# Optimization experiments

Hardware: AMD Instinct MI355X
Metric: run time of the kernel (lower is better)

Reference implementation:

```python
import jax, jax.numpy as jnp
import numpy as np

V, H, B, S, L = 32000, 1024, 128, 256, 2


def setup_inputs() -> dict:
    key = jax.random.key(0)
    ks = jax.random.split(key, 20)
    p = lambda k, shape: (0.02 * jax.random.normal(k, shape)).astype(jnp.float32)
    return {
        "input_ids": jax.random.randint(ks[0], (B,), 0, V),
        "hidden": jax.random.normal(ks[1], (L, B, H), dtype=jnp.float32),
        "encoder_outputs": jax.random.normal(ks[2], (S, B, H), dtype=jnp.float32),
        "embed_table": p(ks[3], (V, H)),
        "W_attn": p(ks[4], (H, 2 * H)),
        "b_attn": p(ks[5], (H,)),
        "v": p(ks[6], (H,)),
        "w_ih0": p(ks[7], (3 * H, H)), "w_hh0": p(ks[8], (3 * H, H)),
        "b_ih0": p(ks[9], (3 * H,)), "b_hh0": p(ks[10], (3 * H,)),
        "w_ih1": p(ks[11], (3 * H, H)), "w_hh1": p(ks[12], (3 * H, H)),
        "b_ih1": p(ks[13], (3 * H,)), "b_hh1": p(ks[14], (3 * H,)),
        "W_concat": p(ks[15], (H, 2 * H)), "b_concat": p(ks[16], (H,)),
        "W_out": p(ks[17], (V, H)), "b_out": p(ks[18], (V,)),
    }


def gru_cell(x, h, w_ih, w_hh, b_ih, b_hh):
    # PyTorch GRU cell: gates order (r, z, n)
    gi = x @ w_ih.T + b_ih  # [B, 3H]
    gh = h @ w_hh.T + b_hh
    ir, iz, inn = jnp.split(gi, 3, axis=-1)
    hr, hz, hn = jnp.split(gh, 3, axis=-1)
    r = jax.nn.sigmoid(ir + hr)
    z = jax.nn.sigmoid(iz + hz)
    n = jnp.tanh(inn + r * hn)
    return (1.0 - z) * n + z * h


def reference(input_ids, hidden, encoder_outputs, embed_table, W_attn, b_attn, v,
              w_ih0, w_hh0, b_ih0, b_hh0, w_ih1, w_hh1, b_ih1, b_hh1,
              W_concat, b_concat, W_out, b_out):
    # embedding lookup (dropout is identity in eval mode)
    x = embed_table[input_ids]  # [B, H]
    # 2-layer GRU, single time step
    h0 = gru_cell(x, hidden[0], w_ih0, w_hh0, b_ih0, b_hh0)
    h1 = gru_cell(h0, hidden[1], w_ih1, w_hh1, b_ih1, b_hh1)
    rnn_out = h1                                   # [B, H]
    new_hidden = jnp.stack([h0, h1], axis=0)       # [L, B, H]
    # Bahdanau-style scorer: energy = Linear(cat(h, enc)); score = v . energy
    h_b = jnp.broadcast_to(rnn_out[None, :, :], encoder_outputs.shape)  # [S, B, H]
    feats = jnp.concatenate([h_b, encoder_outputs], axis=-1)            # [S, B, 2H]
    energy = jnp.einsum('sbe,he->sbh', feats, W_attn) + b_attn          # [S, B, H]
    scores = jnp.einsum('sbh,h->bs', energy, v)                         # [B, S]
    attn_weights = jax.nn.softmax(scores, axis=1)                       # [B, S]
    # context = attn_weights @ encoder_outputs (bmm)
    context = jnp.einsum('bs,sbh->bh', attn_weights, encoder_outputs)   # [B, H]
    concat_in = jnp.concatenate([rnn_out, context], axis=-1)            # [B, 2H]
    concat_out = jnp.tanh(concat_in @ W_concat.T + b_concat)            # [B, H]
    output = concat_out @ W_out.T + b_out                               # [B, V]
    return (output, new_hidden, attn_weights[:, None, :])
```

## Files before the change

kernel.cpp:

```cpp
#include <hip/hip_runtime.h>
#include <cstdint>
#include <cstddef>

typedef __attribute__((ext_vector_type(4))) float f32x4;
typedef __attribute__((ext_vector_type(8))) __bf16 bf16x8;
typedef __attribute__((ext_vector_type(8))) short short8;

__device__ __forceinline__ unsigned short f2bf(float f) {
  unsigned u = __builtin_bit_cast(unsigned, f);
  u += 0x7FFFu + ((u >> 16) & 1u);
  return (unsigned short)(u >> 16);
}
__device__ __forceinline__ unsigned pack2(float a, float b) {
  return (unsigned)f2bf(a) | ((unsigned)f2bf(b) << 16);
}

__device__ __forceinline__ void async16(const void* g, void* l) {
  __builtin_amdgcn_global_load_lds((const __attribute__((address_space(1))) unsigned int*)g,
                                   (__attribute__((address_space(3))) unsigned int*)l, 16, 0, 0);
}

struct GemmArgs {
  const unsigned short* A;
  const float* W;
  const float* bias;
  float* C;
};

template <int BN, int WAVES_M, int WAVES_N>
__device__ __forceinline__ void gemm_body(const GemmArgs g, int bx, int bz, int lda, int ldw,
                                          int N, int Kseg, int seg_stride) {
  constexpr int WM = 128 / WAVES_M, WN = BN / WAVES_N;
  constexpr int MT = WM / 16, NT = WN / 16;
  __shared__ unsigned short a_lds[2][128 * 64];
  __shared__ unsigned short w_lds[2][BN * 64];

  const int kbase = bz * Kseg;
  const int tid = threadIdx.x;
  const int wave = tid >> 6, lane = tid & 63;
  const int quad = lane >> 4, l16 = lane & 15;
  const int n0 = bx * BN;
  const int wm = (wave / WAVES_N) * WM, wn = (wave % WAVES_N) * WN;
  const int niter = Kseg >> 6;

  f32x4 wv[2];

  auto stageA = [&](int k0, int buf) {
#pragma unroll
    for (int i = 0; i < 4; ++i) {
      int chunk = (wave * 4 + i) * 64 + lane;
      int r = chunk >> 3;
      int c = (chunk & 7) ^ (r & 7);
      async16(g.A + (size_t)r * lda + (k0 + c * 8), &a_lds[buf][chunk * 8]);
    }
  };
  auto loadW = [&](int k0) {
    if constexpr (BN == 32) {
      const float* p = g.W + (size_t)(n0 + (tid >> 3)) * ldw + k0 + (tid & 7) * 8;
      wv[0] = *(const f32x4*)p;
      wv[1] = *(const f32x4*)(p + 4);
    } else {
      const float* p = g.W + (size_t)(n0 + (tid >> 4)) * ldw + k0 + ((tid >> 1) & 7) * 8 + (tid & 1) * 4;
      wv[0] = *(const f32x4*)p;
    }
  };
  auto writeW = [&](int buf) {
    if constexpr (BN == 32) {
      int wr = tid >> 3, wc = tid & 7;
      uint4 pk{pack2(wv[0].x, wv[0].y), pack2(wv[0].z, wv[0].w),
               pack2(wv[1].x, wv[1].y), pack2(wv[1].z, wv[1].w)};
      *(uint4*)&w_lds[buf][(wr * 8 + (wc ^ (wr & 7))) * 8] = pk;
    } else {
      int wr = tid >> 4, wc = (tid >> 1) & 7, half = tid & 1;
      uint2 pk{pack2(wv[0].x, wv[0].y), pack2(wv[0].z, wv[0].w)};
      *(uint2*)&w_lds[buf][(wr * 8 + (wc ^ (wr & 7))) * 8 + half * 4] = pk;
    }
  };

  f32x4 acc[MT][NT] = {};

  stageA(kbase, 0);
  loadW(kbase);
  writeW(0);
  __syncthreads();

  for (int ki = 0; ki < niter; ++ki) {
    const int cur = ki & 1;
    const bool more = (ki + 1 < niter);
    if (more) {
      stageA(kbase + (ki + 1) * 64, cur ^ 1);
      loadW(kbase + (ki + 1) * 64);
    }
#pragma unroll
    for (int kh = 0; kh < 2; ++kh) {
      const int c = kh * 4 + quad;
      bf16x8 af[MT], wf[NT];
#pragma unroll
      for (int mt = 0; mt < MT; ++mt) {
        int m = wm + mt * 16 + l16;
        af[mt] = __builtin_bit_cast(bf16x8, *(const short8*)&a_lds[cur][(m * 8 + (c ^ (m & 7))) * 8]);
      }
#pragma unroll
      for (int nt = 0; nt < NT; ++nt) {
        int n = wn + nt * 16 + l16;
        wf[nt] = __builtin_bit_cast(bf16x8, *(const short8*)&w_lds[cur][(n * 8 + (c ^ (n & 7))) * 8]);
      }
#pragma unroll
      for (int mt = 0; mt < MT; ++mt)
#pragma unroll
        for (int nt = 0; nt < NT; ++nt)
          acc[mt][nt] = __builtin_amdgcn_mfma_f32_16x16x32_bf16(af[mt], wf[nt], acc[mt][nt], 0, 0, 0);
    }
    if (more) writeW(cur ^ 1);
    __syncthreads();
  }

  float* C = g.C + (size_t)bz * seg_stride;
#pragma unroll
  for (int mt = 0; mt < MT; ++mt)
#pragma unroll
    for (int nt = 0; nt < NT; ++nt) {
      int n = n0 + wn + nt * 16 + l16;
      float bv = (bz == 0) ? g.bias[n] : 0.f;
#pragma unroll
      for (int r = 0; r < 4; ++r) {
        int m = wm + mt * 16 + quad * 4 + r;
        C[(size_t)m * N + n] = acc[mt][nt][r] + bv;
      }
    }
}

template <int BN, int WAVES_M, int WAVES_N>
__global__ __launch_bounds__(256, 4) void gemm_bt(GemmArgs g0, GemmArgs g1, int lda, int ldw,
                                                  int N, int Kseg, int seg_stride) {
  gemm_body<BN, WAVES_M, WAVES_N>((blockIdx.y == 0) ? g0 : g1, blockIdx.x, blockIdx.z,
                                  lda, ldw, N, Kseg, seg_stride);
}

__device__ __forceinline__ void prep_body(int b, const int* __restrict__ ids,
                                          const float* __restrict__ hidden,
                                          const float* __restrict__ embed,
                                          unsigned short* A0, unsigned short* Hh0,
                                          unsigned short* Hh1) {
  int job = b >> 7, m = b & 127, t = threadIdx.x;
  const float* src;
  unsigned short* dst;
  if (job == 0) { src = embed + (size_t)ids[m] * 1024; dst = A0; }
  else if (job == 1) { src = hidden + (size_t)m * 1024; dst = Hh0; }
  else { src = hidden + 131072 + (size_t)m * 1024; dst = Hh1; }
  f32x4 v = ((const f32x4*)src)[t];
  uint2 pk{pack2(v.x, v.y), pack2(v.z, v.w)};
  *(uint2*)(dst + (size_t)m * 1024 + t * 4) = pk;
}

__device__ __forceinline__ void u2_body(int b, const float* __restrict__ W_attn,
                                        const float* __restrict__ v, float* __restrict__ u2) {
  int eb = b & 3, hc = b >> 2;
  int e = eb * 256 + threadIdx.x;
  float acc = 0.f;
  int h0 = hc * 32;
#pragma unroll 4
  for (int h = h0; h < h0 + 32; ++h) acc += v[h] * W_attn[(size_t)h * 2048 + 1024 + e];
  atomicAdd(u2 + e, acc);
}

__device__ __forceinline__ void scores_body(int b, const float* __restrict__ enc,
                                            const float* __restrict__ u2,
                                            float* __restrict__ sct) {
  int wave = threadIdx.x >> 6, lane = threadIdx.x & 63;
  const f32x4* u4 = (const f32x4*)u2;
  int row0 = (b * 4 + wave) * 4;
  const f32x4* base = (const f32x4*)enc;
  float a[4] = {0.f, 0.f, 0.f, 0.f};
#pragma unroll
  for (int ph = 0; ph < 2; ++ph) {
    f32x4 uv[2], ev[4][2];
#pragma unroll
    for (int p = 0; p < 2; ++p) uv[p] = u4[(ph * 2 + p) * 64 + lane];
#pragma unroll
    for (int r = 0; r < 4; ++r)
#pragma unroll
      for (int p = 0; p < 2; ++p)
        ev[r][p] = base[(size_t)(row0 + r) * 256 + (ph * 2 + p) * 64 + lane];
#pragma unroll
    for (int r = 0; r < 4; ++r)
#pragma unroll
      for (int p = 0; p < 2; ++p)
        a[r] += ev[r][p].x * uv[p].x + ev[r][p].y * uv[p].y + ev[r][p].z * uv[p].z +
                ev[r][p].w * uv[p].w;
  }
#pragma unroll
  for (int r = 0; r < 4; ++r)
#pragma unroll
    for (int off = 32; off > 0; off >>= 1) a[r] += __shfl_down(a[r], off, 64);
  if (lane == 0) {
#pragma unroll
    for (int r = 0; r < 4; ++r) {
      int row = row0 + r;
      sct[(row & 127) * 256 + (row >> 7)] = a[r];
    }
  }
}

__device__ __forceinline__ void softmax_body(int b, const float* __restrict__ sct,
                                             float* __restrict__ attn) {
  __shared__ float wmax[4], wsum[4];
  int t = threadIdx.x;
  int wave = t >> 6, lane = t & 63;
  float sc = sct[b * 256 + t];
  float m = sc;
#pragma unroll
  for (int off = 32; off > 0; off >>= 1) m = fmaxf(m, __shfl_xor(m, off, 64));
  if (lane == 0) wmax[wave] = m;
  __syncthreads();
  float m4 = fmaxf(fmaxf(wmax[0], wmax[1]), fmaxf(wmax[2], wmax[3]));
  float e = __expf(sc - m4);
  float s = e;
#pragma unroll
  for (int off = 32; off > 0; off >>= 1) s += __shfl_xor(s, off, 64);
  if (lane == 0) wsum[wave] = s;
  __syncthreads();
  float tot = (wsum[0] + wsum[1]) + (wsum[2] + wsum[3]);
  attn[b * 256 + t] = e / tot;
}

__device__ __forceinline__ void context_body(int blk, const float* __restrict__ enc,
                                             const float* __restrict__ attn,
                                             unsigned short* __restrict__ catin) {
  __shared__ float sm[256];
  int b = blk >> 2, hc = blk & 3;
  int t = threadIdx.x;
  sm[t] = attn[b * 256 + t];
  __syncthreads();
  int h = hc * 256 + t;
  const float* ep = enc + (size_t)b * 1024 + h;
  float a[16];
#pragma unroll
  for (int i = 0; i < 16; ++i) a[i] = 0.f;
  for (int s0 = 0; s0 < 256; s0 += 16)
#pragma unroll
    for (int i = 0; i < 16; ++i) a[i] += sm[s0 + i] * ep[(size_t)(s0 + i) * 131072];
  float tot = 0.f;
#pragma unroll
  for (int i = 0; i < 16; ++i) tot += a[i];
  catin[(size_t)b * 2048 + 1024 + h] = f2bf(tot);
}

__device__ __forceinline__ void gate_body(int b, const float* __restrict__ gi,
                                          const float* __restrict__ gh,
                                          const float* __restrict__ h_prev,
                                          float* __restrict__ h_out,
                                          unsigned short* __restrict__ h_bf, int bf_ld) {
  constexpr int SEG = 393216;
  int j = threadIdx.x * 4;
  const float* gib = gi + (size_t)b * 3072;
  const float* ghb = gh + (size_t)b * 3072;
  f32x4 ir = *(const f32x4*)(gib + j) + *(const f32x4*)(gib + SEG + j);
  f32x4 iz = *(const f32x4*)(gib + 1024 + j) + *(const f32x4*)(gib + SEG + 1024 + j);
  f32x4 in_ = *(const f32x4*)(gib + 2048 + j) + *(const f32x4*)(gib + SEG + 2048 + j);
  f32x4 hr = *(const f32x4*)(ghb + j) + *(const f32x4*)(ghb + SEG + j);
  f32x4 hz = *(const f32x4*)(ghb + 1024 + j) + *(const f32x4*)(ghb + SEG + 1024 + j);
  f32x4 hn = *(const f32x4*)(ghb + 2048 + j) + *(const f32x4*)(ghb + SEG + 2048 + j);
  f32x4 hp = *(const f32x4*)(h_prev + (size_t)b * 1024 + j);
  f32x4 ho;
#pragma unroll
  for (int c = 0; c < 4; ++c) {
    float r = 1.f / (1.f + __expf(-(ir[c] + hr[c])));
    float z = 1.f / (1.f + __expf(-(iz[c] + hz[c])));
    float n = tanhf(in_[c] + r * hn[c]);
    ho[c] = (1.f - z) * n + z * hp[c];
  }
  *(f32x4*)(h_out + (size_t)b * 1024 + j) = ho;
  uint2 pk{pack2(ho.x, ho.y), pack2(ho.z, ho.w)};
  *(uint2*)(h_bf + (size_t)b * bf_ld + j) = pk;
}

__global__ __launch_bounds__(256) void gru_gate(const float* __restrict__ gi,
                                                const float* __restrict__ gh,
                                                const float* __restrict__ h_prev,
                                                float* __restrict__ h_out,
                                                unsigned short* __restrict__ h_bf, int bf_ld) {
  gate_body(blockIdx.x, gi, gh, h_prev, h_out, h_bf, bf_ld);
}

__global__ __launch_bounds__(256) void cat_fix(const float* __restrict__ part,
                                               unsigned short* __restrict__ catbf) {
  int m = blockIdx.x, j = threadIdx.x * 4;
  const float* p = part + (size_t)m * 1024 + j;
  f32x4 s = *(const f32x4*)p + *(const f32x4*)(p + 131072) + *(const f32x4*)(p + 262144) +
            *(const f32x4*)(p + 393216);
  f32x4 o;
#pragma unroll
  for (int c = 0; c < 4; ++c) o[c] = tanhf(s[c]);
  uint2 pk{pack2(o.x, o.y), pack2(o.z, o.w)};
  *(uint2*)(catbf + (size_t)m * 1024 + j) = pk;
}

__global__ __launch_bounds__(256) void m0_prep_u2(const int* ids, const float* hidden,
                                                  const float* embed, unsigned short* A0,
                                                  unsigned short* Hh0, unsigned short* Hh1,
                                                  const float* W_attn, const float* v,
                                                  float* u2) {
  int b = blockIdx.x;
  if (b < 384) prep_body(b, ids, hidden, embed, A0, Hh0, Hh1);
  else u2_body(b - 384, W_attn, v, u2);
}

__global__ __launch_bounds__(256, 4) void m1_gru0_scores(GemmArgs g0, GemmArgs g1,
                                                         const float* enc, const float* u2,
                                                         float* sct) {
  int b = blockIdx.x;
  if (b < 768) {
    int bx = b % 192, by = (b / 192) & 1, bz = b / 384;
    gemm_body<16, 4, 1>(by ? g1 : g0, bx, bz, 1024, 1024, 3072, 512, 393216);
  } else {
    scores_body(b - 768, enc, u2, sct);
  }
}

__global__ __launch_bounds__(256) void m2_gate0_softmax(const float* gi, const float* gh,
                                                        const float* h_prev, float* h_out,
                                                        unsigned short* h_bf,
                                                        const float* sct, float* attn) {
  int b = blockIdx.x;
  if (b < 128) gate_body(b, gi, gh, h_prev, h_out, h_bf, 1024);
  else softmax_body(b - 128, sct, attn);
}

__global__ __launch_bounds__(256, 4) void m3_gru1_context(GemmArgs g0, GemmArgs g1,
                                                          const float* enc, const float* attn,
                                                          unsigned short* catin) {
  int b = blockIdx.x;
  if (b < 768) {
    int bx = b % 192, by = (b / 192) & 1, bz = b / 384;
    gemm_body<16, 4, 1>(by ? g1 : g0, bx, bz, 1024, 1024, 3072, 512, 393216);
  } else {
    context_body(b - 768, enc, attn, catin);
  }
}

extern "C" void kernel_launch(void* const* d_in, const int* in_sizes, int n_in,
                              void* d_out_, int out_size, void* d_ws, size_t ws_size,
                              hipStream_t stream) {
  const int* ids = (const int*)d_in[0];
  const float* hidden = (const float*)d_in[1];
  const float* enc = (const float*)d_in[2];
  const float* embed = (const float*)d_in[3];
  const float* W_attn = (const float*)d_in[4];
  const float* v = (const float*)d_in[6];
  const float* w_ih0 = (const float*)d_in[7];
  const float* w_hh0 = (const float*)d_in[8];
  const float* b_ih0 = (const float*)d_in[9];
  const float* b_hh0 = (const float*)d_in[10];
  const float* w_ih1 = (const float*)d_in[11];
  const float* w_hh1 = (const float*)d_in[12];
  const float* b_ih1 = (const float*)d_in[13];
  const float* b_hh1 = (const float*)d_in[14];
  const float* W_cat = (const float*)d_in[15];
  const float* b_cat = (const float*)d_in[16];
  const float* W_out = (const float*)d_in[17];
  const float* b_out = (const float*)d_in[18];

  float* out = (float*)d_out_;
  float* h0 = out + 4096000;
  float* h1 = out + 4227072;
  float* attn = out + 4358144;

  float* ws = (float*)d_ws;
  float* gi = ws;
  float* gh = ws + 786432;
  float* u2 = ws + 1572864;
  float* sct = ws + 1573888;
  float* catp = ws + 1606656;
  unsigned short* bfb = (unsigned short*)(ws + 2130944);
  unsigned short* A0 = bfb;
  unsigned short* Hh0 = bfb + 131072;
  unsigned short* Hh1 = bfb + 262144;
  unsigned short* h0bf = bfb + 393216;
  unsigned short* catin = bfb + 524288;
  unsigned short* catbf = bfb + 786432;

  hipMemsetAsync(u2, 0, 1024 * sizeof(float), stream);
  m0_prep_u2<<<512, 256, 0, stream>>>(ids, hidden, embed, A0, Hh0, Hh1, W_attn, v, u2);

  {
    GemmArgs ai{A0, w_ih0, b_ih0, gi}, ah{Hh0, w_hh0, b_hh0, gh};
    m1_gru0_scores<<<2816, 256, 0, stream>>>(ai, ah, enc, u2, sct);
  }

  m2_gate0_softmax<<<256, 256, 0, stream>>>(gi, gh, hidden, h0, h0bf, sct, attn);

  {
    GemmArgs ai{h0bf, w_ih1, b_ih1, gi}, ah{Hh1, w_hh1, b_hh1, gh};
    m3_gru1_context<<<1280, 256, 0, stream>>>(ai, ah, enc, attn, catin);
  }

  gru_gate<<<128, 256, 0, stream>>>(gi, gh, hidden + 131072, h1, catin, 2048);

  {
    GemmArgs ac{catin, W_cat, b_cat, catp};
    gemm_bt<16, 4, 1><<<dim3(64, 1, 4), 256, 0, stream>>>(ac, ac, 2048, 2048, 1024, 512, 131072);
  }
  cat_fix<<<128, 256, 0, stream>>>(catp, catbf);

  {
    GemmArgs ao{catbf, W_out, b_out, out};
    gemm_bt<32, 2, 2><<<dim3(1000, 1, 1), 256, 0, stream>>>(ao, ao, 1024, 1024, 32000, 1024, 0);
  }
}
```

Before: 467.2 us.

## Fuse all stages into one persistent kernel with software grid barriers

Replaces the seven separate kernel launches with a single persistent megakernel. Each stage loops over its former blocks in grid-stride fashion, and stages are separated by atomic-counter grid barriers. Shared memory is pooled across stages, and the grid size is set from the occupancy query. This removes launch gaps and inter-kernel drain, but adds barrier spin cost, relies on every block being co-resident, and keeps the whole grid at the occupancy of the heaviest LDS stage.

```diff
diff --git a/kernel.cpp b/kernel.cpp
--- a/kernel.cpp
+++ b/kernel.cpp
@@ -18,6 +18,19 @@
 __device__ __forceinline__ void async16(const void* g, void* l) {
   __builtin_amdgcn_global_load_lds((const __attribute__((address_space(1))) unsigned int*)g,
                                    (__attribute__((address_space(3))) unsigned int*)l, 16, 0, 0);
+}
+
+__device__ __forceinline__ void grid_barrier(unsigned* bar, int stage, int nblk) {
+  __threadfence();
+  __syncthreads();
+  if (threadIdx.x == 0) {
+    atomicAdd(bar, 1u);
+    const unsigned tgt = (unsigned)stage * (unsigned)nblk;
+    while (__hip_atomic_load(bar, __ATOMIC_ACQUIRE, __HIP_MEMORY_SCOPE_AGENT) < tgt)
+      __builtin_amdgcn_s_sleep(8);
+  }
+  __syncthreads();
+  __threadfence();
 }
 
 struct GemmArgs {
@@ -29,11 +42,11 @@
 
 template <int BN, int WAVES_M, int WAVES_N>
 __device__ __forceinline__ void gemm_body(const GemmArgs g, int bx, int bz, int lda, int ldw,
-                                          int N, int Kseg, int seg_stride) {
+                                          int N, int Kseg, int seg_stride,
+                                          unsigned short* a_pool, unsigned short* w_pool) {
   constexpr int WM = 128 / WAVES_M, WN = BN / WAVES_N;
   constexpr int MT = WM / 16, NT = WN / 16;
-  __shared__ unsigned short a_lds[2][128 * 64];
-  __shared__ unsigned short w_lds[2][BN * 64];
+  constexpr int ASTRIDE = 128 * 64, WSTRIDE = BN * 64;
 
   const int kbase = bz * Kseg;
   const int tid = threadIdx.x;
@@ -46,12 +59,13 @@
   f32x4 wv[2];
 
   auto stageA = [&](int k0, int buf) {
+    unsigned short* dst = a_pool + buf * ASTRIDE;
 #pragma unroll
     for (int i = 0; i < 4; ++i) {
       int chunk = (wave * 4 + i) * 64 + lane;
       int r = chunk >> 3;
       int c = (chunk & 7) ^ (r & 7);
-      async16(g.A + (size_t)r * lda + (k0 + c * 8), &a_lds[buf][chunk * 8]);
+      async16(g.A + (size_t)r * lda + (k0 + c * 8), dst + chunk * 8);
     }
   };
   auto loadW = [&](int k0) {
@@ -65,15 +79,16 @@
     }
   };
   auto writeW = [&](int buf) {
+    unsigned short* dst = w_pool + buf * WSTRIDE;
     if constexpr (BN == 32) {
       int wr = tid >> 3, wc = tid & 7;
       uint4 pk{pack2(wv[0].x, wv[0].y), pack2(wv[0].z, wv[0].w),
                pack2(wv[1].x, wv[1].y), pack2(wv[1].z, wv[1].w)};
-      *(uint4*)&w_lds[buf][(wr * 8 + (wc ^ (wr & 7))) * 8] = pk;
+      *(uint4*)&dst[(wr * 8 + (wc ^ (wr & 7))) * 8] = pk;
     } else {
       int wr = tid >> 4, wc = (tid >> 1) & 7, half = tid & 1;
       uint2 pk{pack2(wv[0].x, wv[0].y), pack2(wv[0].z, wv[0].w)};
-      *(uint2*)&w_lds[buf][(wr * 8 + (wc ^ (wr & 7))) * 8 + half * 4] = pk;
+      *(uint2*)&dst[(wr * 8 + (wc ^ (wr & 7))) * 8 + half * 4] = pk;
     }
   };
 
@@ -91,6 +106,8 @@
       stageA(kbase + (ki + 1) * 64, cur ^ 1);
       loadW(kbase + (ki + 1) * 64);
     }
+    const unsigned short* ab = a_pool + cur * ASTRIDE;
+    const unsigned short* wb = w_pool + cur * WSTRIDE;
 #pragma unroll
     for (int kh = 0; kh < 2; ++kh) {
       const int c = kh * 4 + quad;
@@ -98,12 +115,12 @@
 #pragma unroll
       for (int mt = 0; mt < MT; ++mt) {
         int m = wm + mt * 16 + l16;
-        af[mt] = __builtin_bit_cast(bf16x8, *(const short8*)&a_lds[cur][(m * 8 + (c ^ (m & 7))) * 8]);
+        af[mt] = __builtin_bit_cast(bf16x8, *(const short8*)&ab[(m * 8 + (c ^ (m & 7))) * 8]);
       }
 #pragma unroll
       for (int nt = 0; nt < NT; ++nt) {
         int n = wn + nt * 16 + l16;
-        wf[nt] = __builtin_bit_cast(bf16x8, *(const short8*)&w_lds[cur][(n * 8 + (c ^ (n & 7))) * 8]);
+        wf[nt] = __builtin_bit_cast(bf16x8, *(const short8*)&wb[(n * 8 + (c ^ (n & 7))) * 8]);
       }
 #pragma unroll
       for (int mt = 0; mt < MT; ++mt)
@@ -128,13 +145,6 @@
         C[(size_t)m * N + n] = acc[mt][nt][r] + bv;
       }
     }
-}
-
-template <int BN, int WAVES_M, int WAVES_N>
-__global__ __launch_bounds__(256, 4) void gemm_bt(GemmArgs g0, GemmArgs g1, int lda, int ldw,
-                                                  int N, int Kseg, int seg_stride) {
-  gemm_body<BN, WAVES_M, WAVES_N>((blockIdx.y == 0) ? g0 : g1, blockIdx.x, blockIdx.z,
-                                  lda, ldw, N, Kseg, seg_stride);
 }
 
 __device__ __forceinline__ void prep_body(int b, const int* __restrict__ ids,
@@ -203,8 +213,9 @@
 }
 
 __device__ __forceinline__ void softmax_body(int b, const float* __restrict__ sct,
-                                             float* __restrict__ attn) {
-  __shared__ float wmax[4], wsum[4];
+                                             float* __restrict__ attn, float* sbuf) {
+  float* wmax = sbuf;
+  float* wsum = sbuf + 4;
   int t = threadIdx.x;
   int wave = t >> 6, lane = t & 63;
   float sc = sct[b * 256 + t];
@@ -226,10 +237,10 @@
 
 __device__ __forceinline__ void context_body(int blk, const float* __restrict__ enc,
                                              const float* __restrict__ attn,
-                                             unsigned short* __restrict__ catin) {
-  __shared__ float sm[256];
+                                             unsigned short* __restrict__ catin, float* sm) {
   int b = blk >> 2, hc = blk & 3;
   int t = threadIdx.x;
+  __syncthreads();
   sm[t] = attn[b * 256 + t];
   __syncthreads();
   int h = hc * 256 + t;
@@ -275,17 +286,9 @@
   *(uint2*)(h_bf + (size_t)b * bf_ld + j) = pk;
 }
 
-__global__ __launch_bounds__(256) void gru_gate(const float* __restrict__ gi,
-                                                const float* __restrict__ gh,
-                                                const float* __restrict__ h_prev,
-                                                float* __restrict__ h_out,
-                                                unsigned short* __restrict__ h_bf, int bf_ld) {
-  gate_body(blockIdx.x, gi, gh, h_prev, h_out, h_bf, bf_ld);
-}
-
-__global__ __launch_bounds__(256) void cat_fix(const float* __restrict__ part,
-                                               unsigned short* __restrict__ catbf) {
-  int m = blockIdx.x, j = threadIdx.x * 4;
+__device__ __forceinline__ void catfix_body(int m, const float* __restrict__ part,
+                                            unsigned short* __restrict__ catbf) {
+  int j = threadIdx.x * 4;
   const float* p = part + (size_t)m * 1024 + j;
   f32x4 s = *(const f32x4*)p + *(const f32x4*)(p + 131072) + *(const f32x4*)(p + 262144) +
             *(const f32x4*)(p + 393216);
@@ -296,115 +299,134 @@
   *(uint2*)(catbf + (size_t)m * 1024 + j) = pk;
 }
 
-__global__ __launch_bounds__(256) void m0_prep_u2(const int* ids, const float* hidden,
-                                                  const float* embed, unsigned short* A0,
-                                                  unsigned short* Hh0, unsigned short* Hh1,
-                                                  const float* W_attn, const float* v,
-                                                  float* u2) {
-  int b = blockIdx.x;
-  if (b < 384) prep_body(b, ids, hidden, embed, A0, Hh0, Hh1);
-  else u2_body(b - 384, W_attn, v, u2);
-}
-
-__global__ __launch_bounds__(256, 4) void m1_gru0_scores(GemmArgs g0, GemmArgs g1,
-                                                         const float* enc, const float* u2,
-                                                         float* sct) {
-  int b = blockIdx.x;
-  if (b < 768) {
-    int bx = b % 192, by = (b / 192) & 1, bz = b / 384;
-    gemm_body<16, 4, 1>(by ? g1 : g0, bx, bz, 1024, 1024, 3072, 512, 393216);
-  } else {
-    scores_body(b - 768, enc, u2, sct);
-  }
-}
-
-__global__ __launch_bounds__(256) void m2_gate0_softmax(const float* gi, const float* gh,
-                                                        const float* h_prev, float* h_out,
-                                                        unsigned short* h_bf,
-                                                        const float* sct, float* attn) {
-  int b = blockIdx.x;
-  if (b < 128) gate_body(b, gi, gh, h_prev, h_out, h_bf, 1024);
-  else softmax_body(b - 128, sct, attn);
-}
-
-__global__ __launch_bounds__(256, 4) void m3_gru1_context(GemmArgs g0, GemmArgs g1,
-                                                          const float* enc, const float* attn,
-                                                          unsigned short* catin) {
-  int b = blockIdx.x;
-  if (b < 768) {
-    int bx = b % 192, by = (b / 192) & 1, bz = b / 384;
-    gemm_body<16, 4, 1>(by ? g1 : g0, bx, bz, 1024, 1024, 3072, 512, 393216);
-  } else {
-    context_body(b - 768, enc, attn, catin);
+struct MegaP {
+  const int* ids;
+  const float *hidden, *enc, *embed, *W_attn, *v;
+  const float *w_ih0, *w_hh0, *b_ih0, *b_hh0;
+  const float *w_ih1, *w_hh1, *b_ih1, *b_hh1;
+  const float *W_cat, *b_cat, *W_out, *b_out;
+  float *out, *h0, *h1, *attn;
+  float *gi, *gh, *u2, *sct, *catp;
+  unsigned short *A0, *Hh0, *Hh1, *h0bf, *catin, *catbf;
+  unsigned* bar;
+};
+
+__global__ __launch_bounds__(256, 4) void mega(MegaP p) {
+  __shared__ unsigned short s_a[2 * 128 * 64];
+  __shared__ unsigned short s_w[2 * 32 * 64];
+  const int nblk = gridDim.x;
+  const int bid = blockIdx.x;
+
+  for (int j = bid; j < 512; j += nblk) {
+    if (j < 384) prep_body(j, p.ids, p.hidden, p.embed, p.A0, p.Hh0, p.Hh1);
+    else u2_body(j - 384, p.W_attn, p.v, p.u2);
+  }
+  grid_barrier(p.bar, 1, nblk);
+
+  for (int j = bid; j < 2816; j += nblk) {
+    if (j < 768) {
+      int bx = j % 192, by = (j / 192) & 1, bz = j / 384;
+      GemmArgs g{by ? p.Hh0 : p.A0, by ? p.w_hh0 : p.w_ih0, by ? p.b_hh0 : p.b_ih0,
+                 by ? p.gh : p.gi};
+      gemm_body<16, 4, 1>(g, bx, bz, 1024, 1024, 3072, 512, 393216, s_a, s_w);
+    } else {
+      scores_body(j - 768, p.enc, p.u2, p.sct);
+    }
+  }
+  grid_barrier(p.bar, 2, nblk);
+
+  for (int j = bid; j < 256; j += nblk) {
+    if (j < 128) gate_body(j, p.gi, p.gh, p.hidden, p.h0, p.h0bf, 1024);
+    else softmax_body(j - 128, p.sct, p.attn, (float*)s_w);
+  }
+  grid_barrier(p.bar, 3, nblk);
+
+  for (int j = bid; j < 1280; j += nblk) {
+    if (j < 768) {
+      int bx = j % 192, by = (j / 192) & 1, bz = j / 384;
+      GemmArgs g{by ? p.Hh1 : p.h0bf, by ? p.w_hh1 : p.w_ih1, by ? p.b_hh1 : p.b_ih1,
+                 by ? p.gh : p.gi};
+      gemm_body<16, 4, 1>(g, bx, bz, 1024, 1024, 3072, 512, 393216, s_a, s_w);
+    } else {
+      context_body(j - 768, p.enc, p.attn, p.catin, (float*)s_a);
+    }
+  }
+  grid_barrier(p.bar, 4, nblk);
+
+  for (int j = bid; j < 128; j += nblk)
+    gate_body(j, p.gi, p.gh, p.hidden + 131072, p.h1, p.catin, 2048);
+  grid_barrier(p.bar, 5, nblk);
+
+  for (int j = bid; j < 256; j += nblk) {
+    GemmArgs g{p.catin, p.W_cat, p.b_cat, p.catp};
+    gemm_body<16, 4, 1>(g, j % 64, j / 64, 2048, 2048, 1024, 512, 131072, s_a, s_w);
+  }
+  grid_barrier(p.bar, 6, nblk);
+
+  for (int j = bid; j < 128; j += nblk) catfix_body(j, p.catp, p.catbf);
+  grid_barrier(p.bar, 7, nblk);
+
+  for (int j = bid; j < 1000; j += nblk) {
+    GemmArgs g{p.catbf, p.W_out, p.b_out, p.out};
+    gemm_body<32, 2, 2>(g, j, 0, 1024, 1024, 32000, 1024, 0, s_a, s_w);
   }
 }
 
 extern "C" void kernel_launch(void* const* d_in, const int* in_sizes, int n_in,
                               void* d_out_, int out_size, void* d_ws, size_t ws_size,
                               hipStream_t stream) {
-  const int* ids = (const int*)d_in[0];
-  const float* hidden = (const float*)d_in[1];
-  const float* enc = (const float*)d_in[2];
-  const float* embed = (const float*)d_in[3];
-  const float* W_attn = (const float*)d_in[4];
-  const float* v = (const float*)d_in[6];
-  const float* w_ih0 = (const float*)d_in[7];
-  const float* w_hh0 = (const float*)d_in[8];
-  const float* b_ih0 = (const float*)d_in[9];
-  const float* b_hh0 = (const float*)d_in[10];
-  const float* w_ih1 = (const float*)d_in[11];
-  const float* w_hh1 = (const float*)d_in[12];
-  const float* b_ih1 = (const float*)d_in[13];
-  const float* b_hh1 = (const float*)d_in[14];
-  const float* W_cat = (const float*)d_in[15];
-  const float* b_cat = (const float*)d_in[16];
-  const float* W_out = (const float*)d_in[17];
-  const float* b_out = (const float*)d_in[18];
-
   float* out = (float*)d_out_;
-  float* h0 = out + 4096000;
-  float* h1 = out + 4227072;
-  float* attn = out + 4358144;
-
   float* ws = (float*)d_ws;
-  float* gi = ws;
-  float* gh = ws + 786432;
-  float* u2 = ws + 1572864;
-  float* sct = ws + 1573888;
-  float* catp = ws + 1606656;
+
+  MegaP p;
+  p.ids = (const int*)d_in[0];
+  p.hidden = (const float*)d_in[1];
+  p.enc = (const float*)d_in[2];
+  p.embed = (const float*)d_in[3];
+  p.W_attn = (const float*)d_in[4];
+  p.v = (const float*)d_in[6];
+  p.w_ih0 = (const float*)d_in[7];
+  p.w_hh0 = (const float*)d_in[8];
+  p.b_ih0 = (const float*)d_in[9];
+  p.b_hh0 = (const float*)d_in[10];
+  p.w_ih1 = (const float*)d_in[11];
+  p.w_hh1 = (const float*)d_in[12];
+  p.b_ih1 = (const float*)d_in[13];
+  p.b_hh1 = (const float*)d_in[14];
+  p.W_cat = (const float*)d_in[15];
+  p.b_cat = (const float*)d_in[16];
+  p.W_out = (const float*)d_in[17];
+  p.b_out = (const float*)d_in[18];
+
+  p.out = out;
+  p.h0 = out + 4096000;
+  p.h1 = out + 4227072;
+  p.attn = out + 4358144;
+
+  p.gi = ws;
+  p.gh = ws + 786432;
+  p.u2 = ws + 1572864;
+  p.sct = ws + 1573888;
+  p.catp = ws + 1606656;
   unsigned short* bfb = (unsigned short*)(ws + 2130944);
-  unsigned short* A0 = bfb;
-  unsigned short* Hh0 = bfb + 131072;
-  unsigned short* Hh1 = bfb + 262144;
-  unsigned short* h0bf = bfb + 393216;
-  unsigned short* catin = bfb + 524288;
-  unsigned short* catbf = bfb + 786432;
-
-  hipMemsetAsync(u2, 0, 1024 * sizeof(float), stream);
-  m0_prep_u2<<<512, 256, 0, stream>>>(ids, hidden, embed, A0, Hh0, Hh1, W_attn, v, u2);
-
-  {
-    GemmArgs ai{A0, w_ih0, b_ih0, gi}, ah{Hh0, w_hh0, b_hh0, gh};
-    m1_gru0_scores<<<2816, 256, 0, stream>>>(ai, ah, enc, u2, sct);
-  }
-
-  m2_gate0_softmax<<<256, 256, 0, stream>>>(gi, gh, hidden, h0, h0bf, sct, attn);
-
-  {
-    GemmArgs ai{h0bf, w_ih1, b_ih1, gi}, ah{Hh1, w_hh1, b_hh1, gh};
-    m3_gru1_context<<<1280, 256, 0, stream>>>(ai, ah, enc, attn, catin);
-  }
-
-  gru_gate<<<128, 256, 0, stream>>>(gi, gh, hidden + 131072, h1, catin, 2048);
-
-  {
-    GemmArgs ac{catin, W_cat, b_cat, catp};
-    gemm_bt<16, 4, 1><<<dim3(64, 1, 4), 256, 0, stream>>>(ac, ac, 2048, 2048, 1024, 512, 131072);
-  }
-  cat_fix<<<128, 256, 0, stream>>>(catp, catbf);
-
-  {
-    GemmArgs ao{catbf, W_out, b_out, out};
-    gemm_bt<32, 2, 2><<<dim3(1000, 1, 1), 256, 0, stream>>>(ao, ao, 1024, 1024, 32000, 1024, 0);
-  }
-}
+  p.A0 = bfb;
+  p.Hh0 = bfb + 131072;
+  p.Hh1 = bfb + 262144;
+  p.h0bf = bfb + 393216;
+  p.catin = bfb + 524288;
+  p.catbf = bfb + 786432;
+  p.bar = (unsigned*)(ws + 4000000);
+
+  static int nblk = 0;
+  if (nblk == 0) {
+    int mb = 0;
+    if (hipOccupancyMaxActiveBlocksPerMultiprocessor(&mb, mega, 256, 0) != hipSuccess || mb < 1)
+      mb = 1;
+    long g = 256L * mb;
+    nblk = (int)(g > 1024 ? 1024 : g);
+  }
+
+  hipMemsetAsync(p.u2, 0, 1024 * sizeof(float), stream);
+  hipMemsetAsync(p.bar, 0, sizeof(unsigned), stream);
+  mega<<<nblk, 256, 0, stream>>>(p);
+}
```

After: 1.329 ms. 2.84x slower.
